# Performance work log

Measured on AMD Instinct MI355X. Metric: run time of the kernel, lower is better.

Reference implementation:

```python
import jax, jax.numpy as jnp
import numpy as np

D, H = 1024, 8
HD = D // H           # head_dim = 128
M1 = 64               # att_mid_dim[1]
ALPHA = 1.3           # CELU alpha
EPS = 1e-5            # GroupNorm eps


def celu(x):
    return jnp.where(x > 0, x, ALPHA * jnp.expm1(x / ALPHA))


def group_norm(x, gamma, beta):
    # torch.nn.GroupNorm(H, D) on 2D input [N, D]: normalize within each group of HD channels
    N, C = x.shape
    xg = x.reshape(N, H, C // H)
    mu = xg.mean(-1, keepdims=True)
    var = xg.var(-1, keepdims=True)
    xn = ((xg - mu) * jax.lax.rsqrt(var + EPS)).reshape(N, C)
    return xn * gamma + beta


def branch(x, W, b, gamma, beta):
    # Linear -> CELU -> GroupNorm
    return group_norm(celu(x @ W + b), gamma, beta)


def setup_inputs() -> dict:
    key = jax.random.key(0)
    ks = jax.random.split(key, 24)
    B, M = 64, 1024
    s = 0.02
    inp = {
        "query": jax.random.normal(ks[0], (B, D), jnp.float32),
        "key": jax.random.normal(ks[1], (B, M, D), jnp.float32),
        "mask": jnp.ones((B, M), jnp.float32),
        "value1": jax.random.normal(ks[2], (B, D), jnp.float32),
        "value2": jax.random.normal(ks[3], (B, M, D), jnp.float32),
    }
    # four Linear+GroupNorm branches
    for i, name in enumerate(["q", "k", "v1", "v2"]):
        inp[f"W{name}"] = jax.random.normal(ks[4 + i], (D, D), jnp.float32) * s
        inp[f"b{name}"] = jnp.zeros((D,), jnp.float32)
        inp[f"g{name}"] = jnp.ones((D,), jnp.float32)
        inp[f"gb{name}"] = jnp.zeros((D,), jnp.float32)
    # SCAttention params: basic Linear(HD->M1), last Linear(M1->1), last2 Linear(M1->HD)
    inp["Wb"] = jax.random.normal(ks[10], (HD, M1), jnp.float32) * s
    inp["bb"] = jnp.zeros((M1,), jnp.float32)
    inp["Wl"] = jax.random.normal(ks[11], (M1, 1), jnp.float32) * s
    inp["bl"] = jnp.zeros((1,), jnp.float32)
    inp["Wl2"] = jax.random.normal(ks[12], (M1, HD), jnp.float32) * s
    inp["bl2"] = jnp.zeros((HD,), jnp.float32)
    return inp


def reference(query, key, mask, value1, value2,
              Wq, bq, gq, gbq, Wk, bk, gk, gbk,
              Wv1, bv1, gv1, gbv1, Wv2, bv2, gv2, gbv2,
              Wb, bb, Wl, bl, Wl2, bl2):
    B = query.shape[0]
    q = branch(query, Wq, bq, gq, gbq).reshape(B, H, HD)           # [B,H,HD]
    v1 = branch(value1, Wv1, bv1, gv1, gbv1).reshape(B, H, HD)     # [B,H,HD]
    k = branch(key.reshape(-1, D), Wk, bk, gk, gbk)
    k = k.reshape(B, -1, H, HD).transpose(0, 2, 1, 3)              # [B,H,M,HD]
    v2 = branch(value2.reshape(-1, D), Wv2, bv2, gv2, gbv2)
    v2 = v2.reshape(B, -1, H, HD).transpose(0, 2, 1, 3)            # [B,H,M,HD]

    attn_map = q[:, :, None, :] * k                                # Hadamard, [B,H,M,HD]

    # SCAttention (eval mode, dropout off)
    am = jax.nn.relu(attn_map @ Wb + bb)                           # [B,H,M,M1]
    mask_e = mask[:, None, :, None]                                # [B,1,M,1]
    am_pool = (am * mask_e).sum(-2) / mask_e.sum(-2)               # [B,H,M1]
    alpha_spatial = (am @ Wl + bl)[..., 0]                         # [B,H,M]
    alpha_channel = jax.nn.sigmoid(am_pool @ Wl2 + bl2)            # [B,H,HD]
    alpha_spatial = jnp.where(mask[:, None, :] == 0, -1e9, alpha_spatial)
    alpha_spatial = jax.nn.softmax(alpha_spatial, axis=-1)
    pooled_v2 = jnp.einsum('bhm,bhmd->bhd', alpha_spatial, v2)     # [B,H,HD]
    attn = v1 * pooled_v2 * alpha_channel                          # [B,H,HD]
    return attn.reshape(B, H * HD)
```

## Files before the change

kernel.cpp:

```cpp
#include <hip/hip_runtime.h>

typedef unsigned short u16;
typedef __attribute__((ext_vector_type(8))) short s16x8;
typedef __attribute__((ext_vector_type(8))) unsigned short u16x8;
typedef __attribute__((ext_vector_type(4))) float f32x4;

#define AS1 __attribute__((address_space(1)))
#define AS3 __attribute__((address_space(3)))

__device__ __forceinline__ float bf2f(u16 u) {
  union { unsigned u; float f; } x; x.u = ((unsigned)u) << 16; return x.f;
}
__device__ __forceinline__ u16 f2bf(float f) {
  union { float f; unsigned u; } x; x.f = f;
  unsigned r = x.u + 0x7fffu + ((x.u >> 16) & 1u);
  return (u16)(r >> 16);
}
__device__ __forceinline__ float celu_f(float x) {
  return x > 0.f ? x : 1.3f * expm1f(x * (1.0f / 1.3f));
}

__global__ __launch_bounds__(256) void transpose2_bf16(
    const float* __restrict__ W0, u16* __restrict__ WT0,
    const float* __restrict__ W1, u16* __restrict__ WT1)
{
  __shared__ float tile[32][33];
  const int bx = blockIdx.x;
  const int sel = blockIdx.y >> 5;
  const int by = blockIdx.y & 31;
  const float* W = sel ? W1 : W0;
  u16* WT = sel ? WT1 : WT0;
  const int tx = threadIdx.x, ty = threadIdx.y;
#pragma unroll
  for (int i = ty; i < 32; i += 8)
    tile[i][tx] = W[(by * 32 + i) * 1024 + bx * 32 + tx];
  __syncthreads();
#pragma unroll
  for (int i = ty; i < 32; i += 8)
    WT[(bx * 32 + i) * 1024 + by * 32 + tx] = f2bf(tile[tx][i]);
}

__global__ __launch_bounds__(256) void transpose_bf16(
    const float* __restrict__ W, u16* __restrict__ WT, int R, int C)
{
  __shared__ float tile[32][33];
  const int bx = blockIdx.x, by = blockIdx.y;
  const int tx = threadIdx.x, ty = threadIdx.y;
#pragma unroll
  for (int i = ty; i < 32; i += 8)
    tile[i][tx] = W[(by * 32 + i) * C + bx * 32 + tx];
  __syncthreads();
#pragma unroll
  for (int i = ty; i < 32; i += 8)
    WT[(bx * 32 + i) * R + by * 32 + tx] = f2bf(tile[tx][i]);
}

__global__ __launch_bounds__(128) void branch_small2(
    const float* __restrict__ X0, const float* __restrict__ W0,
    const float* __restrict__ b0, const float* __restrict__ g0,
    const float* __restrict__ be0, float* __restrict__ o0,
    const float* __restrict__ X1, const float* __restrict__ W1,
    const float* __restrict__ b1, const float* __restrict__ g1,
    const float* __restrict__ be1, float* __restrict__ o1)
{
  const int bid = blockIdx.x;
  const int sel = bid >> 9;
  const float* X = sel ? X1 : X0;  const float* W = sel ? W1 : W0;
  const float* bias = sel ? b1 : b0; const float* gamma = sel ? g1 : g0;
  const float* beta = sel ? be1 : be0; float* out = sel ? o1 : o0;
  const int b = (bid & 511) >> 3, grp = bid & 7;
  const int t = threadIdx.x;
  __shared__ float xs[1024];
  __shared__ float r1[2], r2[2];
  for (int i = t; i < 1024; i += 128) xs[i] = X[b * 1024 + i];
  __syncthreads();
  const int col = grp * 128 + t;
  const float* wp = W + col;
  float a0 = 0.f, a1 = 0.f, a2 = 0.f, a3 = 0.f;
  for (int k = 0; k < 1024; k += 4) {
    a0 += xs[k]     * wp[(k)     * 1024];
    a1 += xs[k + 1] * wp[(k + 1) * 1024];
    a2 += xs[k + 2] * wp[(k + 2) * 1024];
    a3 += xs[k + 3] * wp[(k + 3) * 1024];
  }
  float x = (a0 + a1) + (a2 + a3) + bias[col];
  float c = celu_f(x);
  float s1 = c, s2 = c * c;
#pragma unroll
  for (int m = 1; m < 64; m <<= 1) { s1 += __shfl_xor(s1, m); s2 += __shfl_xor(s2, m); }
  const int w = t >> 6;
  if ((t & 63) == 0) { r1[w] = s1; r2[w] = s2; }
  __syncthreads();
  float t1 = r1[0] + r1[1], t2 = r2[0] + r2[1];
  float mean = t1 * 0.0078125f;
  float var  = t2 * 0.0078125f - mean * mean;
  float inv  = rsqrtf(var + 1e-5f);
  out[b * 1024 + col] = (c - mean) * inv * gamma[col] + beta[col];
}

__global__ void
__attribute__((amdgpu_flat_work_group_size(512, 512), amdgpu_waves_per_eu(2, 2)))
gemm256f(
    const float* __restrict__ A32, const u16* __restrict__ WT,
    const float* __restrict__ bias, const float* __restrict__ gamma,
    const float* __restrict__ beta, u16* __restrict__ Cout)
{
  __shared__ __align__(16) char lds_raw[143360];

  const int tid  = threadIdx.x;
  const int lane = tid & 63;
  const int w    = tid >> 6;
  const int wr   = w >> 2, wc = w & 3;
  const int lg   = lane >> 4, ln = lane & 15;

  const int bid = blockIdx.x;
  const int v   = (bid & 7) * 128 + (bid >> 3);
  const int mt  = v >> 2, nt = v & 3;

#define AQOFF(wr2, h, sl) ((((wr2) * 2 + (h)) * 2 + (sl)) * 8192)
#define BOFF(sl)          (65536 + (sl) * 32768)

  const int trow = tid >> 3;
  const int gsw  = ((tid & 7) ^ (trow & 7)) * 8;
  const u16* bS0  = WT + (long)(nt * 256 +   0 + trow) * 1024 + gsw;
  const u16* bS1  = WT + (long)(nt * 256 +  64 + trow) * 1024 + gsw;
  const u16* bS2  = WT + (long)(nt * 256 + 128 + trow) * 1024 + gsw;
  const u16* bS3  = WT + (long)(nt * 256 + 192 + trow) * 1024 + gsw;

#define B_STAGE(sl, kt)                                                         \
  { __builtin_amdgcn_global_load_lds((const AS1 void*)(bS0 + (kt) * 64),        \
        (AS3 void*)(lds_raw + BOFF(sl) +     0 + w * 1024), 16, 0, 0);          \
    __builtin_amdgcn_global_load_lds((const AS1 void*)(bS1 + (kt) * 64),        \
        (AS3 void*)(lds_raw + BOFF(sl) +  8192 + w * 1024), 16, 0, 0);          \
    __builtin_amdgcn_global_load_lds((const AS1 void*)(bS2 + (kt) * 64),        \
        (AS3 void*)(lds_raw + BOFF(sl) + 16384 + w * 1024), 16, 0, 0);          \
    __builtin_amdgcn_global_load_lds((const AS1 void*)(bS3 + (kt) * 64),        \
        (AS3 void*)(lds_raw + BOFF(sl) + 24576 + w * 1024), 16, 0, 0); }

  const int arow = tid >> 3;
  const int acc_ = tid & 7;
  const float* aR[4];
  int awb[4];
#pragma unroll
  for (int s = 0; s < 4; ++s) {
    int row_l = s * 64 + arow;
    aR[s] = A32 + (long)(mt * 256 + row_l) * 1024 + acc_ * 8;
    int q  = row_l >> 6;
    int rq = row_l & 63;
    awb[s] = q * 16384 + rq * 128 + ((acc_ ^ (rq & 7)) * 16);
  }

#define A_LOAD(AV, s, kt)                                                       \
  { AV[2*(s)]   = *(const f32x4*)(aR[s] + (kt) * 64);                           \
    AV[2*(s)+1] = *(const f32x4*)(aR[s] + (kt) * 64 + 4); }
#define A_WRITE(AV, s, sl)                                                      \
  { u16x8 tt;                                                                   \
    _Pragma("unroll")                                                           \
    for (int e = 0; e < 4; ++e) { tt[e] = f2bf(AV[2*(s)][e]);                   \
                                  tt[4+e] = f2bf(AV[2*(s)+1][e]); }             \
    *(u16x8*)(lds_raw + awb[s] + (sl) * 8192) = tt; }

  int aoff0[4], aoff1[4], boff0[4], boff1[4];
#pragma unroll
  for (int la = 0; la < 4; ++la) {
    int rq = la * 16 + ln;
    aoff0[la] = rq * 128 + (((0 * 4 + lg) ^ (ln & 7)) * 16);
    aoff1[la] = rq * 128 + (((1 * 4 + lg) ^ (ln & 7)) * 16);
  }
#pragma unroll
  for (int j = 0; j < 4; ++j) {
    int nl = wc * 64 + j * 16 + ln;
    boff0[j] = nl * 128 + (((0 * 4 + lg) ^ (ln & 7)) * 16);
    boff1[j] = nl * 128 + (((1 * 4 + lg) ^ (ln & 7)) * 16);
  }

  f32x4 acc[8][4] = {};

#define MFMA_SET(IB, BF)                                                        \
    _Pragma("unroll")                                                           \
    for (int la = 0; la < 4; ++la)                                              \
      _Pragma("unroll")                                                         \
      for (int j = 0; j < 4; ++j)                                               \
        acc[(IB) + la][j] = __builtin_amdgcn_mfma_f32_16x16x32_bf16(            \
            afv[la], BF[j], acc[(IB) + la][j], 0, 0, 0);

#define KITER(T, STG)                                                           \
  {                                                                             \
    const int slot = (T) & 1, nslot = slot ^ 1;                                 \
    const char* aqb0 = lds_raw + AQOFF(wr, 0, slot);                            \
    const char* aqb1 = lds_raw + AQOFF(wr, 1, slot);                            \
    const char* bqb  = lds_raw + BOFF(slot);                                    \
    s16x8 bfr[4], afv[4];                                                       \
    f32x4 av[8];                                                                \
                      \
    _Pragma("unroll")                                                           \
    for (int la = 0; la < 4; ++la) afv[la] = *(const s16x8*)(aqb0 + aoff0[la]); \
    _Pragma("unroll")                                                           \
    for (int j = 0; j < 4; ++j) bfr[j] = *(const s16x8*)(bqb + boff0[j]);       \
    if (STG) { B_STAGE(nslot, (T) + 1);                                         \
               A_LOAD(av, 0, (T) + 1) A_LOAD(av, 1, (T) + 1) }                  \
    __builtin_amdgcn_s_barrier();                                               \
    asm volatile("s_waitcnt lgkmcnt(0)" ::);                                    \
    __builtin_amdgcn_sched_barrier(0);                                          \
    __builtin_amdgcn_s_setprio(1);                                              \
    MFMA_SET(0, bfr)                                                            \
    __builtin_amdgcn_s_setprio(0);                                              \
    __builtin_amdgcn_s_barrier();                                               \
    __builtin_amdgcn_sched_barrier(0);                                          \
                                      \
    _Pragma("unroll")                                                           \
    for (int la = 0; la < 4; ++la) afv[la] = *(const s16x8*)(aqb1 + aoff0[la]); \
    if (STG) { A_LOAD(av, 2, (T) + 1) A_LOAD(av, 3, (T) + 1) }                  \
    __builtin_amdgcn_s_barrier();                                               \
    asm volatile("s_waitcnt lgkmcnt(0)" ::);                                    \
    __builtin_amdgcn_sched_barrier(0);                                          \
    __builtin_amdgcn_s_setprio(1);                                              \
    MFMA_SET(4, bfr)                                                            \
    __builtin_amdgcn_s_setprio(0);                                              \
    __builtin_amdgcn_s_barrier();                                               \
    __builtin_amdgcn_sched_barrier(0);                                          \
                        \
    _Pragma("unroll")                                                           \
    for (int la = 0; la < 4; ++la) afv[la] = *(const s16x8*)(aqb0 + aoff1[la]); \
    _Pragma("unroll")                                                           \
    for (int j = 0; j < 4; ++j) bfr[j] = *(const s16x8*)(bqb + boff1[j]);       \
    if (STG) { A_WRITE(av, 0, nslot) A_WRITE(av, 1, nslot) }                    \
    __builtin_amdgcn_s_barrier();                                               \
    asm volatile("s_waitcnt lgkmcnt(0)" ::);                                    \
    __builtin_amdgcn_sched_barrier(0);                                          \
    __builtin_amdgcn_s_setprio(1);                                              \
    MFMA_SET(0, bfr)                                                            \
    __builtin_amdgcn_s_setprio(0);                                              \
    __builtin_amdgcn_s_barrier();                                               \
    __builtin_amdgcn_sched_barrier(0);                                          \
                         \
    _Pragma("unroll")                                                           \
    for (int la = 0; la < 4; ++la) afv[la] = *(const s16x8*)(aqb1 + aoff1[la]); \
    if (STG) { A_WRITE(av, 2, nslot) A_WRITE(av, 3, nslot) }                    \
    __builtin_amdgcn_s_barrier();                                               \
    asm volatile("s_waitcnt lgkmcnt(0)" ::);                                    \
    __builtin_amdgcn_sched_barrier(0);                                          \
    __builtin_amdgcn_s_setprio(1);                                              \
    MFMA_SET(4, bfr)                                                            \
    __builtin_amdgcn_s_setprio(0);                                              \
    __syncthreads();   \
    __builtin_amdgcn_sched_barrier(0);                                          \
  }

  {
    B_STAGE(0, 0);
    f32x4 av[8];
    A_LOAD(av, 0, 0) A_LOAD(av, 1, 0) A_LOAD(av, 2, 0) A_LOAD(av, 3, 0)
    A_WRITE(av, 0, 0) A_WRITE(av, 1, 0) A_WRITE(av, 2, 0) A_WRITE(av, 3, 0)
    __syncthreads();
  }

  for (int t = 0; t < 15; ++t)
    KITER(t, 1)
  KITER(15, 0)

#undef KITER
#undef MFMA_SET
#undef A_LOAD
#undef A_WRITE
#undef B_STAGE
#undef AQOFF
#undef BOFF

  u16*   Csh = (u16*)lds_raw;
  float* red = (float*)(lds_raw + 135168);

  float bsv[4];
#pragma unroll
  for (int j = 0; j < 4; ++j) bsv[j] = bias[nt * 256 + wc * 64 + j * 16 + ln];

#pragma unroll
  for (int i = 0; i < 8; ++i) {
    float s1[4] = {0.f, 0.f, 0.f, 0.f}, s2[4] = {0.f, 0.f, 0.f, 0.f};
#pragma unroll
    for (int j = 0; j < 4; ++j) {
#pragma unroll
      for (int r = 0; r < 4; ++r) {
        float c = celu_f(acc[i][j][r] + bsv[j]);
        s1[r] += c; s2[r] += c * c;
        int rl = wr * 128 + i * 16 + 4 * lg + r;
        Csh[rl * 264 + wc * 64 + j * 16 + ln] = f2bf(c);
      }
    }
#pragma unroll
    for (int r = 0; r < 4; ++r) {
#pragma unroll
      for (int m = 1; m < 16; m <<= 1) {
        s1[r] += __shfl_xor(s1[r], m); s2[r] += __shfl_xor(s2[r], m);
      }
      if (ln == 0) {
        int rl = wr * 128 + i * 16 + 4 * lg + r;
        red[(rl * 4 + wc) * 2 + 0] = s1[r];
        red[(rl * 4 + wc) * 2 + 1] = s2[r];
      }
    }
  }
  __syncthreads();

  const int rsub = tid >> 5;
  const int cseg = (tid & 31) * 8;
  const int g2   = (cseg >> 7) * 2;
#pragma unroll 4
  for (int s = 0; s < 16; ++s) {
    int row_l = s * 16 + rsub;
    float s1t = red[(row_l * 4 + g2) * 2 + 0] + red[(row_l * 4 + g2 + 1) * 2 + 0];
    float s2t = red[(row_l * 4 + g2) * 2 + 1] + red[(row_l * 4 + g2 + 1) * 2 + 1];
    float mean = s1t * 0.0078125f;
    float var  = s2t * 0.0078125f - mean * mean;
    float inv  = rsqrtf(var + 1e-5f);
    u16x8 cv = *(const u16x8*)(Csh + row_l * 264 + cseg);
    int col0 = nt * 256 + cseg;
    f32x4 g0 = *(const f32x4*)(gamma + col0);
    f32x4 g1 = *(const f32x4*)(gamma + col0 + 4);
    f32x4 b0 = *(const f32x4*)(beta + col0);
    f32x4 b1 = *(const f32x4*)(beta + col0 + 4);
    u16x8 ov;
#pragma unroll
    for (int e = 0; e < 4; ++e) {
      ov[e]     = f2bf((bf2f(cv[e])     - mean) * inv * g0[e] + b0[e]);
      ov[4 + e] = f2bf((bf2f(cv[4 + e]) - mean) * inv * g1[e] + b1[e]);
    }
    *(u16x8*)(Cout + (long)(mt * 256 + row_l) * 1024 + col0) = ov;
  }
}

__global__ __launch_bounds__(256) void stage2(
    const float* __restrict__ qb, const float* __restrict__ v1b,
    const u16* __restrict__ kbuf, const u16* __restrict__ v2buf,
    const u16* __restrict__ wbT, const float* __restrict__ bb,
    const float* __restrict__ Wl, const float* __restrict__ bl,
    const float* __restrict__ Wl2, const float* __restrict__ bl2,
    const float* __restrict__ mask, float* __restrict__ out)
{
  const int bh = blockIdx.x, b = bh >> 3, h = bh & 7;
  const int tid = threadIdx.x, lane = tid & 63, w = tid >> 6;
  const int lg = lane >> 4, ln = lane & 15;

  __shared__ float s_arr[1024];
  __shared__ float pool_l[4][64];
  __shared__ float poolf[64];
  __shared__ float ach[128];
  __shared__ float psum2[4][128];
  __shared__ float rmsk[4], rmax[4], rsum[4];

  float qv[4][8];
#pragma unroll
  for (int ks = 0; ks < 4; ++ks)
#pragma unroll
    for (int e = 0; e < 8; ++e)
      qv[ks][e] = qb[b * 1024 + h * 128 + ks * 32 + lg * 8 + e];

  s16x8 bfr[4][4];
#pragma unroll
  for (int nj = 0; nj < 4; ++nj)
#pragma unroll
    for (int ks = 0; ks < 4; ++ks)
      bfr[nj][ks] = *(const s16x8*)(&wbT[(nj * 16 + ln) * 128 + ks * 32 + lg * 8]);

  float wlv[4], bbv[4];
#pragma unroll
  for (int nj = 0; nj < 4; ++nj) { wlv[nj] = Wl[nj * 16 + ln]; bbv[nj] = bb[nj * 16 + ln]; }

  float mpart = 0.f;
  for (int m = tid; m < 1024; m += 256) mpart += mask[b * 1024 + m];

  float poolacc[4] = {0.f, 0.f, 0.f, 0.f};

  for (int c = 0; c < 16; ++c) {
    const int m0 = w * 256 + c * 16;
    f32x4 amacc[4] = {};
#pragma unroll
    for (int ks = 0; ks < 4; ++ks) {
      const u16* kp = kbuf + (long)(b * 1024 + m0 + ln) * 1024 + h * 128 + ks * 32 + lg * 8;
      u16x8 kw = *(const u16x8*)kp;
      s16x8 af;
#pragma unroll
      for (int e = 0; e < 8; ++e) af[e] = (short)f2bf(bf2f(kw[e]) * qv[ks][e]);
#pragma unroll
      for (int nj = 0; nj < 4; ++nj)
        amacc[nj] = __builtin_amdgcn_mfma_f32_16x16x32_bf16(af, bfr[nj][ks], amacc[nj], 0, 0, 0);
    }
    float mrow[4];
#pragma unroll
    for (int r = 0; r < 4; ++r) mrow[r] = mask[b * 1024 + m0 + lg * 4 + r];
    float sp[4] = {0.f, 0.f, 0.f, 0.f};
#pragma unroll
    for (int nj = 0; nj < 4; ++nj)
#pragma unroll
      for (int r = 0; r < 4; ++r) {
        float a = fmaxf(amacc[nj][r] + bbv[nj], 0.f);
        poolacc[nj] += a * mrow[r];
        sp[r] += a * wlv[nj];
      }
#pragma unroll
    for (int m = 1; m < 16; m <<= 1)
#pragma unroll
      for (int r = 0; r < 4; ++r) sp[r] += __shfl_xor(sp[r], m);
    if (ln == 0) {
#pragma unroll
      for (int r = 0; r < 4; ++r) s_arr[m0 + lg * 4 + r] = sp[r] + bl[0];
    }
  }
#pragma unroll
  for (int m = 16; m < 64; m <<= 1)
#pragma unroll
    for (int nj = 0; nj < 4; ++nj) poolacc[nj] += __shfl_xor(poolacc[nj], m);
  if (lg == 0) {
#pragma unroll
    for (int nj = 0; nj < 4; ++nj) pool_l[w][nj * 16 + ln] = poolacc[nj];
  }
#pragma unroll
  for (int m = 1; m < 64; m <<= 1) mpart += __shfl_xor(mpart, m);
  if (lane == 0) rmsk[w] = mpart;
  __syncthreads();
  const float msum = rmsk[0] + rmsk[1] + rmsk[2] + rmsk[3];
  if (tid < 64) poolf[tid] = pool_l[0][tid] + pool_l[1][tid] + pool_l[2][tid] + pool_l[3][tid];
  float lmax = -3.0e38f;
  for (int m = tid; m < 1024; m += 256) {
    float sv = (mask[b * 1024 + m] == 0.f) ? -1.0e9f : s_arr[m];
    s_arr[m] = sv;
    lmax = fmaxf(lmax, sv);
  }
#pragma unroll
  for (int m = 1; m < 64; m <<= 1) lmax = fmaxf(lmax, __shfl_xor(lmax, m));
  if (lane == 0) rmax[w] = lmax;
  __syncthreads();
  const float gmax = fmaxf(fmaxf(rmax[0], rmax[1]), fmaxf(rmax[2], rmax[3]));
  float lsum = 0.f;
  for (int m = tid; m < 1024; m += 256) {
    float e = expf(s_arr[m] - gmax);
    s_arr[m] = e;
    lsum += e;
  }
#pragma unroll
  for (int m = 1; m < 64; m <<= 1) lsum += __shfl_xor(lsum, m);
  if (lane == 0) rsum[w] = lsum;
  if (tid < 128) {
    float a = 0.f;
    for (int cc = 0; cc < 64; ++cc) a += poolf[cc] * Wl2[cc * 128 + tid];
    a = a / msum + bl2[tid];
    ach[tid] = 1.f / (1.f + expf(-a));
  }
  __syncthreads();
  const float gsum = rsum[0] + rsum[1] + rsum[2] + rsum[3];

  float pacc[8] = {0.f, 0.f, 0.f, 0.f, 0.f, 0.f, 0.f, 0.f};
  const u16* vbase = v2buf + (long)(b * 1024 + w * 256) * 1024 + h * 128 + ln * 8;
#pragma unroll 4
  for (int i = 0; i < 64; ++i) {
    const int mrow = i * 4 + lg;
    u16x8 vv = *(const u16x8*)(vbase + (long)mrow * 1024);
    float s = s_arr[w * 256 + mrow];
#pragma unroll
    for (int e = 0; e < 8; ++e) pacc[e] += s * bf2f(vv[e]);
  }
#pragma unroll
  for (int e = 0; e < 8; ++e) {
    pacc[e] += __shfl_xor(pacc[e], 16);
    pacc[e] += __shfl_xor(pacc[e], 32);
  }
  if (lg == 0) {
    f32x4 p0 = {pacc[0], pacc[1], pacc[2], pacc[3]};
    f32x4 p1 = {pacc[4], pacc[5], pacc[6], pacc[7]};
    *(f32x4*)&psum2[w][ln * 8]     = p0;
    *(f32x4*)&psum2[w][ln * 8 + 4] = p1;
  }
  __syncthreads();
  if (tid < 128) {
    float pooled = (psum2[0][tid] + psum2[1][tid] + psum2[2][tid] + psum2[3][tid]) / gsum;
    out[b * 1024 + h * 128 + tid] = v1b[b * 1024 + h * 128 + tid] * pooled * ach[tid];
  }
}

extern "C" void kernel_launch(void* const* d_in, const int* in_sizes, int n_in,
                              void* d_out, int out_size, void* d_ws, size_t ws_size,
                              hipStream_t stream)
{
  (void)in_sizes; (void)n_in; (void)out_size; (void)ws_size;
  const float* query  = (const float*)d_in[0];
  const float* key    = (const float*)d_in[1];
  const float* mask   = (const float*)d_in[2];
  const float* value1 = (const float*)d_in[3];
  const float* value2 = (const float*)d_in[4];
  const float* Wq  = (const float*)d_in[5];
  const float* bq  = (const float*)d_in[6];
  const float* gq  = (const float*)d_in[7];
  const float* gbq = (const float*)d_in[8];
  const float* Wk  = (const float*)d_in[9];
  const float* bk  = (const float*)d_in[10];
  const float* gk  = (const float*)d_in[11];
  const float* gbk = (const float*)d_in[12];
  const float* Wv1  = (const float*)d_in[13];
  const float* bv1  = (const float*)d_in[14];
  const float* gv1  = (const float*)d_in[15];
  const float* gbv1 = (const float*)d_in[16];
  const float* Wv2  = (const float*)d_in[17];
  const float* bv2  = (const float*)d_in[18];
  const float* gv2  = (const float*)d_in[19];
  const float* gbv2 = (const float*)d_in[20];
  const float* Wb  = (const float*)d_in[21];
  const float* bb  = (const float*)d_in[22];
  const float* Wl  = (const float*)d_in[23];
  const float* bl  = (const float*)d_in[24];
  const float* Wl2 = (const float*)d_in[25];
  const float* bl2 = (const float*)d_in[26];
  float* out = (float*)d_out;

  char* ws = (char*)d_ws;
  const long SZ128 = 134217728L;
  u16*   k_out  = (u16*)(ws);
  u16*   v2_out = (u16*)(ws + SZ128);
  char*  wbase  = ws + 2 * SZ128;
  u16*   WkT    = (u16*)(wbase);
  u16*   Wv2T   = (u16*)(wbase + 2097152L);
  u16*   WbT    = (u16*)(wbase + 2L * 2097152L);
  float* qbuf   = (float*)(wbase + 2L * 2097152L + 32768L);
  float* v1buf  = (float*)(wbase + 2L * 2097152L + 32768L + 262144L);

  dim3 tb(32, 8);
  transpose2_bf16<<<dim3(32, 64), tb, 0, stream>>>(Wk, WkT, Wv2, Wv2T);
  transpose_bf16<<<dim3(2, 4), tb, 0, stream>>>(Wb, WbT, 128, 64);

  branch_small2<<<1024, 128, 0, stream>>>(query, Wq, bq, gq, gbq, qbuf,
                                          value1, Wv1, bv1, gv1, gbv1, v1buf);

  gemm256f<<<1024, 512, 0, stream>>>(key,    WkT,  bk,  gk,  gbk,  k_out);
  gemm256f<<<1024, 512, 0, stream>>>(value2, Wv2T, bv2, gv2, gbv2, v2_out);

  stage2<<<512, 256, 0, stream>>>(qbuf, v1buf, k_out, v2_out, WbT,
                                  bb, Wl, bl, Wl2, bl2, mask, out);
}
```

Baseline: 730.8 us.

## Prefetch A tiles two iterations ahead with ping-pong register buffers

The GEMM main loop now keeps two sets of register buffers for the fp32 A tile and issues global loads for iteration t+2 while writing iteration t+1's data into LDS. This gives global loads a whole iteration of latency to hide. The end-of-iteration __syncthreads is replaced by an explicit vmcnt wait plus s_barrier, so only the older loads must finish. The cost is more VGPRs (a second 8-element f32x4 buffer) at a fixed two waves per EU, which could cause spills, and the hand-set vmcnt counts must match the number of outstanding loads.

```diff
diff --git a/kernel.cpp b/kernel.cpp
--- a/kernel.cpp
+++ b/kernel.cpp
@@ -100,7 +100,7 @@
 
 __global__ void
 __attribute__((amdgpu_flat_work_group_size(512, 512), amdgpu_waves_per_eu(2, 2)))
-gemm256f(
+gemm256f2(
     const float* __restrict__ A32, const u16* __restrict__ WT,
     const float* __restrict__ bias, const float* __restrict__ gamma,
     const float* __restrict__ beta, u16* __restrict__ Cout)
@@ -175,6 +175,7 @@
   }
 
   f32x4 acc[8][4] = {};
+  f32x4 avA[8], avB[8];
 
 #define MFMA_SET(IB, BF)                                                        \
     _Pragma("unroll")                                                           \
@@ -184,21 +185,20 @@
         acc[(IB) + la][j] = __builtin_amdgcn_mfma_f32_16x16x32_bf16(            \
             afv[la], BF[j], acc[(IB) + la][j], 0, 0, 0);
 
-#define KITER(T, STG)                                                           \
+#define KITER(T, CUR, NXT, DO_STG, DO_LOAD, EW)                                 \
   {                                                                             \
     const int slot = (T) & 1, nslot = slot ^ 1;                                 \
     const char* aqb0 = lds_raw + AQOFF(wr, 0, slot);                            \
     const char* aqb1 = lds_raw + AQOFF(wr, 1, slot);                            \
     const char* bqb  = lds_raw + BOFF(slot);                                    \
     s16x8 bfr[4], afv[4];                                                       \
-    f32x4 av[8];                                                                \
-                      \
+           \
     _Pragma("unroll")                                                           \
     for (int la = 0; la < 4; ++la) afv[la] = *(const s16x8*)(aqb0 + aoff0[la]); \
     _Pragma("unroll")                                                           \
     for (int j = 0; j < 4; ++j) bfr[j] = *(const s16x8*)(bqb + boff0[j]);       \
-    if (STG) { B_STAGE(nslot, (T) + 1);                                         \
-               A_LOAD(av, 0, (T) + 1) A_LOAD(av, 1, (T) + 1) }                  \
+    if (DO_STG) B_STAGE(nslot, (T) + 1);                                        \
+    if (DO_LOAD) { A_LOAD(NXT, 0, (T) + 2) A_LOAD(NXT, 1, (T) + 2) }            \
     __builtin_amdgcn_s_barrier();                                               \
     asm volatile("s_waitcnt lgkmcnt(0)" ::);                                    \
     __builtin_amdgcn_sched_barrier(0);                                          \
@@ -207,10 +207,10 @@
     __builtin_amdgcn_s_setprio(0);                                              \
     __builtin_amdgcn_s_barrier();                                               \
     __builtin_amdgcn_sched_barrier(0);                                          \
-                                      \
+                           \
     _Pragma("unroll")                                                           \
     for (int la = 0; la < 4; ++la) afv[la] = *(const s16x8*)(aqb1 + aoff0[la]); \
-    if (STG) { A_LOAD(av, 2, (T) + 1) A_LOAD(av, 3, (T) + 1) }                  \
+    if (DO_LOAD) { A_LOAD(NXT, 2, (T) + 2) A_LOAD(NXT, 3, (T) + 2) }            \
     __builtin_amdgcn_s_barrier();                                               \
     asm volatile("s_waitcnt lgkmcnt(0)" ::);                                    \
     __builtin_amdgcn_sched_barrier(0);                                          \
@@ -219,12 +219,12 @@
     __builtin_amdgcn_s_setprio(0);                                              \
     __builtin_amdgcn_s_barrier();                                               \
     __builtin_amdgcn_sched_barrier(0);                                          \
-                        \
+                 \
     _Pragma("unroll")                                                           \
     for (int la = 0; la < 4; ++la) afv[la] = *(const s16x8*)(aqb0 + aoff1[la]); \
     _Pragma("unroll")                                                           \
     for (int j = 0; j < 4; ++j) bfr[j] = *(const s16x8*)(bqb + boff1[j]);       \
-    if (STG) { A_WRITE(av, 0, nslot) A_WRITE(av, 1, nslot) }                    \
+    if (DO_STG) { A_WRITE(CUR, 0, nslot) A_WRITE(CUR, 1, nslot) }               \
     __builtin_amdgcn_s_barrier();                                               \
     asm volatile("s_waitcnt lgkmcnt(0)" ::);                                    \
     __builtin_amdgcn_sched_barrier(0);                                          \
@@ -233,31 +233,36 @@
     __builtin_amdgcn_s_setprio(0);                                              \
     __builtin_amdgcn_s_barrier();                                               \
     __builtin_amdgcn_sched_barrier(0);                                          \
-                         \
+     \
     _Pragma("unroll")                                                           \
     for (int la = 0; la < 4; ++la) afv[la] = *(const s16x8*)(aqb1 + aoff1[la]); \
-    if (STG) { A_WRITE(av, 2, nslot) A_WRITE(av, 3, nslot) }                    \
+    if (DO_STG) { A_WRITE(CUR, 2, nslot) A_WRITE(CUR, 3, nslot) }               \
     __builtin_amdgcn_s_barrier();                                               \
     asm volatile("s_waitcnt lgkmcnt(0)" ::);                                    \
     __builtin_amdgcn_sched_barrier(0);                                          \
     __builtin_amdgcn_s_setprio(1);                                              \
     MFMA_SET(4, bfr)                                                            \
     __builtin_amdgcn_s_setprio(0);                                              \
-    __syncthreads();   \
+    if (DO_STG) { asm volatile("s_waitcnt vmcnt(" EW ")" ::);                   \
+                  __builtin_amdgcn_sched_barrier(0); }                          \
+    __builtin_amdgcn_s_barrier();                                               \
     __builtin_amdgcn_sched_barrier(0);                                          \
   }
 
   {
     B_STAGE(0, 0);
-    f32x4 av[8];
-    A_LOAD(av, 0, 0) A_LOAD(av, 1, 0) A_LOAD(av, 2, 0) A_LOAD(av, 3, 0)
-    A_WRITE(av, 0, 0) A_WRITE(av, 1, 0) A_WRITE(av, 2, 0) A_WRITE(av, 3, 0)
+    A_LOAD(avA, 0, 0) A_LOAD(avA, 1, 0) A_LOAD(avA, 2, 0) A_LOAD(avA, 3, 0)
+    A_WRITE(avA, 0, 0) A_WRITE(avA, 1, 0) A_WRITE(avA, 2, 0) A_WRITE(avA, 3, 0)
+    A_LOAD(avA, 0, 1) A_LOAD(avA, 1, 1) A_LOAD(avA, 2, 1) A_LOAD(avA, 3, 1)
     __syncthreads();
   }
 
-  for (int t = 0; t < 15; ++t)
-    KITER(t, 1)
-  KITER(15, 0)
+  for (int t = 0; t < 14; t += 2) {
+    KITER(t,     avA, avB, 1, 1, "8")
+    KITER(t + 1, avB, avA, 1, 1, "8")
+  }
+  KITER(14, avA, avB, 1, 0, "0")
+  KITER(15, avB, avA, 0, 0, "0")
 
 #undef KITER
 #undef MFMA_SET
@@ -529,8 +534,8 @@
   branch_small2<<<1024, 128, 0, stream>>>(query, Wq, bq, gq, gbq, qbuf,
                                           value1, Wv1, bv1, gv1, gbv1, v1buf);
 
-  gemm256f<<<1024, 512, 0, stream>>>(key,    WkT,  bk,  gk,  gbk,  k_out);
-  gemm256f<<<1024, 512, 0, stream>>>(value2, Wv2T, bv2, gv2, gbv2, v2_out);
+  gemm256f2<<<1024, 512, 0, stream>>>(key,    WkT,  bk,  gk,  gbk,  k_out);
+  gemm256f2<<<1024, 512, 0, stream>>>(value2, Wv2T, bv2, gv2, gbv2, v2_out);
 
   stage2<<<512, 256, 0, stream>>>(qbuf, v1buf, k_out, v2_out, WbT,
                                   bb, Wl, bl, Wl2, bl2, mask, out);
```

After: 869.6 us. 19.0% more time.
